# Kernel optimization log

Measured on AMD Instinct MI355X. Metric: run time of the kernel, lower is better.

The kernel has to match this reference:

```python
import jax, jax.numpy as jnp
import numpy as np

INPUT_SIZE = 2
HIDDEN = 64
NUM_CLASSES = 64
B = 4096
T = 512


def setup_inputs() -> dict:
    key = jax.random.key(0)
    ks = jax.random.split(key, 12)
    s_in = 1.0 / np.sqrt(HIDDEN)
    inp = {
        "x": jax.random.normal(ks[0], (B, INPUT_SIZE, T, 1), dtype=jnp.float32),
        # LSTMCell params (torch layout: [4H, in], gate order i,f,g,o)
        "W_ih": jax.random.uniform(ks[1], (4 * HIDDEN, INPUT_SIZE), minval=-s_in, maxval=s_in),
        "W_hh": jax.random.uniform(ks[2], (4 * HIDDEN, HIDDEN), minval=-s_in, maxval=s_in),
        "b_ih": jax.random.uniform(ks[3], (4 * HIDDEN,), minval=-s_in, maxval=s_in),
        "b_hh": jax.random.uniform(ks[4], (4 * HIDDEN,), minval=-s_in, maxval=s_in),
        # ODE cell f_node: Linear(H,H) -> Tanh -> Linear(H,H)
        "W1": jax.random.uniform(ks[5], (HIDDEN, HIDDEN), minval=-s_in, maxval=s_in),
        "b1": jax.random.uniform(ks[6], (HIDDEN,), minval=-s_in, maxval=s_in),
        "W2": jax.random.uniform(ks[7], (HIDDEN, HIDDEN), minval=-s_in, maxval=s_in),
        "b2": jax.random.uniform(ks[8], (HIDDEN,), minval=-s_in, maxval=s_in),
        # output projection fc
        "Wf": jax.random.uniform(ks[9], (NUM_CLASSES, HIDDEN), minval=-s_in, maxval=s_in),
        "bf": jax.random.uniform(ks[10], (NUM_CLASSES,), minval=-s_in, maxval=s_in),
    }
    return inp


def reference(x, W_ih, W_hh, b_ih, b_hh, W1, b1, W2, b2, Wf, bf):
    # x: [B, input_size, T, 1] -> [T, B, input_size] for scan over time
    xs = jnp.transpose(x[..., 0], (2, 0, 1))
    b = xs.shape[1]
    H = W_hh.shape[1]
    dt = jnp.float32(1.0 / 3.0)  # ts = ones(B), 3 fixed Euler steps of ts/3

    def f_node(h):
        return jnp.tanh(h @ W1.T + b1) @ W2.T + b2

    def step(carry, xt):
        h, c = carry
        gates = xt @ W_ih.T + h @ W_hh.T + (b_ih + b_hh)  # [B, 4H]
        i, f, g, o = jnp.split(gates, 4, axis=-1)
        c = jax.nn.sigmoid(f) * c + jax.nn.sigmoid(i) * jnp.tanh(g)
        h = jax.nn.sigmoid(o) * jnp.tanh(c)
        # fixed-Euler ODE solve: 3 steps
        for _ in range(3):
            h = h + dt * f_node(h)
        return (h, c), h @ Wf.T + bf

    h0 = jnp.zeros((b, H), dtype=x.dtype)
    c0 = jnp.zeros((b, H), dtype=x.dtype)
    _, outs = jax.lax.scan(step, (h0, c0), xs)  # outs: [T, B, num_classes]
    return jnp.transpose(outs, (1, 0, 2))  # [B, T, num_classes]
```

## Files before the change

### kernel.cpp

```cpp
#include <hip/hip_runtime.h>


#define TT 512
#define DT 0.33333334f

#define OFF_M  0
#define OFF_N  4096
#define OFF_P  20480
#define OFF_K1 24576
#define OFF_CG 24640
#define OFF_C2 24896

typedef _Float16 half8 __attribute__((ext_vector_type(8)));
typedef float f32x4 __attribute__((ext_vector_type(4)));

__device__ __forceinline__ float fsig(float x) {
  return __builtin_amdgcn_rcpf(1.0f + __expf(-x));
}
__device__ __forceinline__ float ftanh(float x) {
  return 2.0f * __builtin_amdgcn_rcpf(1.0f + __expf(-2.0f * x)) - 1.0f;
}

__global__ void prep(const float* __restrict__ Whh, const float* __restrict__ W1,
                     const float* __restrict__ W2, const float* __restrict__ b2,
                     const float* __restrict__ Wf, const float* __restrict__ bf,
                     float* __restrict__ ws) {
  int id = (int)blockIdx.x * 256 + (int)threadIdx.x;
  if (id < 4096) {
    int j = id >> 6, k = id & 63;
    float s = 0.f;
    for (int l = 0; l < 64; ++l) s += W1[j * 64 + l] * W2[l * 64 + k];
    ws[OFF_M + id] = DT * s;
  } else if (id < 20480) {
    int e = id - 4096; int gr = e >> 6, k = e & 63;
    float s = 0.f;
    for (int l = 0; l < 64; ++l) s += Whh[gr * 64 + l] * W2[l * 64 + k];
    ws[OFF_N + e] = DT * s;
  } else if (id < 24576) {
    int e = id - 20480; int j = e >> 6, k = e & 63;
    float s = 0.f;
    for (int l = 0; l < 64; ++l) s += Wf[j * 64 + l] * W2[l * 64 + k];
    ws[OFF_P + e] = DT * s;
  } else if (id < 24640) {
    int j = id - 24576;
    float s = 0.f;
    for (int l = 0; l < 64; ++l) s += W1[j * 64 + l] * b2[l];
    ws[OFF_K1 + j] = DT * s;
  } else if (id < 24896) {
    int gr = id - 24640;
    float s = 0.f;
    for (int l = 0; l < 64; ++l) s += Whh[gr * 64 + l] * b2[l];
    ws[OFF_CG + gr] = 3.0f * DT * s;
  } else if (id < 24960) {
    int j = id - 24896;
    float s = 0.f;
    for (int l = 0; l < 64; ++l) s += Wf[j * 64 + l] * b2[l];
    ws[OFF_C2 + j] = 3.0f * DT * s + bf[j];
  }
}

__device__ __forceinline__ half8 rdA(const _Float16* plane, int off) {
  return *(const half8*)(plane + off);
}

__global__ void __launch_bounds__(256, 1)
odelstm(const float* __restrict__ X, const float* __restrict__ Wih,
        const float* __restrict__ Whh, const float* __restrict__ bih,
        const float* __restrict__ bhh, const float* __restrict__ W1,
        const float* __restrict__ b1, const float* __restrict__ Wf,
        const float* __restrict__ ws, float* __restrict__ OUT)
{
  __shared__ __align__(16) _Float16 sh[5 * 1024];

  const int tid = (int)threadIdx.x;
  const int w = tid >> 6;
  const int l = tid & 63;
  const int q = l >> 4;
  const int p = l & 15;
  const int j = (w << 4) | p;
  const int row0 = (int)blockIdx.x << 4;

  half8 Bhh[4][2], Bw1[2], Bm[2], Bn[4][2], Bp[2], Bof[2];
  #pragma unroll
  for (int g = 0; g < 4; ++g) {
    #pragma unroll
    for (int kt = 0; kt < 2; ++kt) {
      const float* s  = Whh + ((g << 6) | j) * 64 + (kt << 5) + (q << 3);
      const float* sn = ws + OFF_N + (((g << 6) | j) << 6) + (kt << 5) + (q << 3);
      half8 v, vn;
      #pragma unroll
      for (int i = 0; i < 8; ++i) { v[i] = (_Float16)s[i]; vn[i] = (_Float16)sn[i]; }
      Bhh[g][kt] = v; Bn[g][kt] = vn;
    }
  }
  #pragma unroll
  for (int kt = 0; kt < 2; ++kt) {
    const float* s1 = W1 + j * 64 + (kt << 5) + (q << 3);
    const float* sm = ws + OFF_M + (j << 6) + (kt << 5) + (q << 3);
    const float* sp = ws + OFF_P + (j << 6) + (kt << 5) + (q << 3);
    const float* sf = Wf + j * 64 + (kt << 5) + (q << 3);
    half8 v1, vm, vp, vf;
    #pragma unroll
    for (int i = 0; i < 8; ++i) {
      v1[i] = (_Float16)s1[i]; vm[i] = (_Float16)sm[i];
      vp[i] = (_Float16)sp[i]; vf[i] = (_Float16)sf[i];
    }
    Bw1[kt] = v1; Bm[kt] = vm; Bp[kt] = vp; Bof[kt] = vf;
  }

  float bias0[4], biasL[4], wx0[4], wx1[4];
  #pragma unroll
  for (int g = 0; g < 4; ++g) {
    int gr = (g << 6) | j;
    bias0[g] = bih[gr] + bhh[gr];
    biasL[g] = bias0[g] + ws[OFF_CG + gr];
    wx0[g] = Wih[gr * 2];
    wx1[g] = Wih[gr * 2 + 1];
  }
  const float b1c = b1[j];
  const float k1c = ws[OFF_K1 + j];
  const float c2c = ws[OFF_C2 + j];

  int waddr[4];
  #pragma unroll
  for (int r = 0; r < 4; ++r) {
    int row = (q << 2) | r;
    waddr[r] = row * 64 + (((j >> 3) ^ (row & 7)) << 3) + (j & 7);
  }
  int roff0 = p * 64 + (((q) ^ (p & 7)) << 3);
  int roff1 = p * 64 + (((4 | q) ^ (p & 7)) << 3);

  const float* xp[4];
  float* outp[4];
  #pragma unroll
  for (int r = 0; r < 4; ++r) {
    int rb = row0 + ((q << 2) | r);
    xp[r]   = X + rb * 2 * TT;
    outp[r] = OUT + (rb * TT) * 64 + j;
  }

  float x0[4], x1[4];
  #pragma unroll
  for (int r = 0; r < 4; ++r) { x0[r] = xp[r][0]; x1[r] = xp[r][TT]; }

  f32x4 acc[4];
  #pragma unroll
  for (int g = 0; g < 4; ++g)
    #pragma unroll
    for (int r = 0; r < 4; ++r)
      acc[g][r] = bias0[g] + x0[r] * wx0[g] + x1[r] * wx1[g];

  float c[4] = {0.f, 0.f, 0.f, 0.f};

  for (int t = 0; t < TT; ++t) {
    _Float16* Hpl = sh + ((t & 1) << 10);
    _Float16* T0p = sh + 2048;
    _Float16* T1p = sh + 3072;
    _Float16* Spp = sh + 4096;

    float hd[4];
    #pragma unroll
    for (int r = 0; r < 4; ++r) {
      float ig = fsig(acc[0][r]);
      float fg = fsig(acc[1][r]);
      float gg = ftanh(acc[2][r]);
      float og = fsig(acc[3][r]);
      c[r]  = fg * c[r] + ig * gg;
      hd[r] = og * ftanh(c[r]);
      Hpl[waddr[r]] = (_Float16)hd[r];
    }
    __syncthreads();

    half8 hf0 = rdA(Hpl, roff0);
    half8 hf1 = rdA(Hpl, roff1);
    f32x4 aa = {b1c, b1c, b1c, b1c};
    aa = __builtin_amdgcn_mfma_f32_16x16x32_f16(hf0, Bw1[0], aa, 0, 0, 0);
    aa = __builtin_amdgcn_mfma_f32_16x16x32_f16(hf1, Bw1[1], aa, 0, 0, 0);

    int tn = (t + 1 < TT) ? t + 1 : t;
    float nx0[4], nx1[4];
    #pragma unroll
    for (int r = 0; r < 4; ++r) { nx0[r] = xp[r][tn]; nx1[r] = xp[r][TT + tn]; }

    float t0s[4];
    #pragma unroll
    for (int r = 0; r < 4; ++r) {
      t0s[r] = ftanh(aa[r]);
      T0p[waddr[r]] = (_Float16)t0s[r];
    }
    __syncthreads();
    half8 t0f0 = rdA(T0p, roff0);
    half8 t0f1 = rdA(T0p, roff1);
    f32x4 a1 = {aa[0] + k1c, aa[1] + k1c, aa[2] + k1c, aa[3] + k1c};
    a1 = __builtin_amdgcn_mfma_f32_16x16x32_f16(t0f0, Bm[0], a1, 0, 0, 0);
    a1 = __builtin_amdgcn_mfma_f32_16x16x32_f16(t0f1, Bm[1], a1, 0, 0, 0);

    float t1s[4];
    #pragma unroll
    for (int r = 0; r < 4; ++r) {
      t1s[r] = ftanh(a1[r]);
      T1p[waddr[r]] = (_Float16)t1s[r];
    }
    __syncthreads();
    half8 t1f0 = rdA(T1p, roff0);
    half8 t1f1 = rdA(T1p, roff1);
    f32x4 a2 = {a1[0] + k1c, a1[1] + k1c, a1[2] + k1c, a1[3] + k1c};
    a2 = __builtin_amdgcn_mfma_f32_16x16x32_f16(t1f0, Bm[0], a2, 0, 0, 0);
    a2 = __builtin_amdgcn_mfma_f32_16x16x32_f16(t1f1, Bm[1], a2, 0, 0, 0);

    #pragma unroll
    for (int r = 0; r < 4; ++r) {
      float Sv = t0s[r] + t1s[r] + ftanh(a2[r]);
      Spp[waddr[r]] = (_Float16)Sv;
    }
    __syncthreads();

    half8 sf0 = rdA(Spp, roff0);
    half8 sf1 = rdA(Spp, roff1);

    #pragma unroll
    for (int g = 0; g < 4; ++g) {
      #pragma unroll
      for (int r = 0; r < 4; ++r)
        acc[g][r] = biasL[g] + nx0[r] * wx0[g] + nx1[r] * wx1[g];
      acc[g] = __builtin_amdgcn_mfma_f32_16x16x32_f16(hf0, Bhh[g][0], acc[g], 0, 0, 0);
      acc[g] = __builtin_amdgcn_mfma_f32_16x16x32_f16(hf1, Bhh[g][1], acc[g], 0, 0, 0);
      acc[g] = __builtin_amdgcn_mfma_f32_16x16x32_f16(sf0, Bn[g][0],  acc[g], 0, 0, 0);
      acc[g] = __builtin_amdgcn_mfma_f32_16x16x32_f16(sf1, Bn[g][1],  acc[g], 0, 0, 0);
    }

    f32x4 oa = {c2c, c2c, c2c, c2c};
    oa = __builtin_amdgcn_mfma_f32_16x16x32_f16(hf0, Bof[0], oa, 0, 0, 0);
    oa = __builtin_amdgcn_mfma_f32_16x16x32_f16(hf1, Bof[1], oa, 0, 0, 0);
    oa = __builtin_amdgcn_mfma_f32_16x16x32_f16(sf0, Bp[0],  oa, 0, 0, 0);
    oa = __builtin_amdgcn_mfma_f32_16x16x32_f16(sf1, Bp[1],  oa, 0, 0, 0);

    #pragma unroll
    for (int r = 0; r < 4; ++r) {
      outp[r][0] = oa[r];
      outp[r] += 64;
    }

    #pragma unroll
    for (int r = 0; r < 4; ++r) { x0[r] = nx0[r]; x1[r] = nx1[r]; }
  }
}

extern "C" void kernel_launch(void* const* d_in, const int* in_sizes, int n_in,
                              void* d_out, int out_size, void* d_ws, size_t ws_size,
                              hipStream_t stream) {
  const float* X   = (const float*)d_in[0];
  const float* Wih = (const float*)d_in[1];
  const float* Whh = (const float*)d_in[2];
  const float* bih = (const float*)d_in[3];
  const float* bhh = (const float*)d_in[4];
  const float* W1  = (const float*)d_in[5];
  const float* b1  = (const float*)d_in[6];
  const float* W2  = (const float*)d_in[7];
  const float* b2  = (const float*)d_in[8];
  const float* Wf  = (const float*)d_in[9];
  const float* bf  = (const float*)d_in[10];
  float* OUT = (float*)d_out;
  float* ws  = (float*)d_ws;

  hipLaunchKernelGGL(prep, dim3(98), dim3(256), 0, stream,
                     Whh, W1, W2, b2, Wf, bf, ws);

  int B = in_sizes[0] / (2 * TT);
  dim3 grid(B / 16), block(256);
  hipLaunchKernelGGL(odelstm, grid, block, 0, stream,
                     X, Wih, Whh, bih, bhh, W1, b1, Wf, ws, OUT);
}
```

Before: 1.190 ms.

## Halve rows per block and run two blocks per CU to hide recurrence latency

Each block now handles 8 batch rows instead of 16, so twice as many blocks are launched, and launch bounds allow two blocks per CU. The 16-row MFMA tiles stay the same size: the unused rows come from zero-initialised shared memory and zeroed accumulator lanes. The aim is to interleave two independent serial recurrence chains on each CU, hiding MFMA, LDS and barrier latency. In exchange, half of each MFMA's work is padding and weight registers are loaded per block twice as often.

```diff
diff --git a/kernel.cpp b/kernel.cpp
--- a/kernel.cpp
+++ b/kernel.cpp
@@ -63,7 +63,7 @@
   return *(const half8*)(plane + off);
 }
 
-__global__ void __launch_bounds__(256, 1)
+__global__ void __launch_bounds__(256, 2)
 odelstm(const float* __restrict__ X, const float* __restrict__ Wih,
         const float* __restrict__ Whh, const float* __restrict__ bih,
         const float* __restrict__ bhh, const float* __restrict__ W1,
@@ -78,7 +78,7 @@
   const int q = l >> 4;
   const int p = l & 15;
   const int j = (w << 4) | p;
-  const int row0 = (int)blockIdx.x << 4;
+  const int row0 = (int)blockIdx.x << 3;
 
   half8 Bhh[4][2], Bw1[2], Bm[2], Bn[4][2], Bp[2], Bof[2];
   #pragma unroll
@@ -121,36 +121,41 @@
   const float k1c = ws[OFF_K1 + j];
   const float c2c = ws[OFF_C2 + j];
 
-  int waddr[4];
-  #pragma unroll
-  for (int r = 0; r < 4; ++r) {
+  int waddr[2];
+  #pragma unroll
+  for (int r = 0; r < 2; ++r) {
     int row = (q << 2) | r;
     waddr[r] = row * 64 + (((j >> 3) ^ (row & 7)) << 3) + (j & 7);
   }
   int roff0 = p * 64 + (((q) ^ (p & 7)) << 3);
   int roff1 = p * 64 + (((4 | q) ^ (p & 7)) << 3);
 
-  const float* xp[4];
-  float* outp[4];
-  #pragma unroll
-  for (int r = 0; r < 4; ++r) {
-    int rb = row0 + ((q << 2) | r);
+  const float* xp[2];
+  float* outp[2];
+  #pragma unroll
+  for (int r = 0; r < 2; ++r) {
+    int rb = row0 + ((q << 1) | r);
     xp[r]   = X + rb * 2 * TT;
     outp[r] = OUT + (rb * TT) * 64 + j;
   }
 
-  float x0[4], x1[4];
-  #pragma unroll
-  for (int r = 0; r < 4; ++r) { x0[r] = xp[r][0]; x1[r] = xp[r][TT]; }
+  for (int i = tid; i < 5 * 1024; i += 256) sh[i] = (_Float16)0.f;
+
+  float x0[2], x1[2];
+  #pragma unroll
+  for (int r = 0; r < 2; ++r) { x0[r] = xp[r][0]; x1[r] = xp[r][TT]; }
 
   f32x4 acc[4];
   #pragma unroll
-  for (int g = 0; g < 4; ++g)
-    #pragma unroll
-    for (int r = 0; r < 4; ++r)
-      acc[g][r] = bias0[g] + x0[r] * wx0[g] + x1[r] * wx1[g];
-
-  float c[4] = {0.f, 0.f, 0.f, 0.f};
+  for (int g = 0; g < 4; ++g) {
+    acc[g][0] = bias0[g] + x0[0] * wx0[g] + x1[0] * wx1[g];
+    acc[g][1] = bias0[g] + x0[1] * wx0[g] + x1[1] * wx1[g];
+    acc[g][2] = 0.f; acc[g][3] = 0.f;
+  }
+
+  float c[2] = {0.f, 0.f};
+
+  __syncthreads();
 
   for (int t = 0; t < TT; ++t) {
     _Float16* Hpl = sh + ((t & 1) << 10);
@@ -158,16 +163,15 @@
     _Float16* T1p = sh + 3072;
     _Float16* Spp = sh + 4096;
 
-    float hd[4];
-    #pragma unroll
-    for (int r = 0; r < 4; ++r) {
+    #pragma unroll
+    for (int r = 0; r < 2; ++r) {
       float ig = fsig(acc[0][r]);
       float fg = fsig(acc[1][r]);
       float gg = ftanh(acc[2][r]);
       float og = fsig(acc[3][r]);
-      c[r]  = fg * c[r] + ig * gg;
-      hd[r] = og * ftanh(c[r]);
-      Hpl[waddr[r]] = (_Float16)hd[r];
+      c[r] = fg * c[r] + ig * gg;
+      float hv = og * ftanh(c[r]);
+      Hpl[waddr[r]] = (_Float16)hv;
     }
     __syncthreads();
 
@@ -178,38 +182,38 @@
     aa = __builtin_amdgcn_mfma_f32_16x16x32_f16(hf1, Bw1[1], aa, 0, 0, 0);
 
     int tn = (t + 1 < TT) ? t + 1 : t;
-    float nx0[4], nx1[4];
-    #pragma unroll
-    for (int r = 0; r < 4; ++r) { nx0[r] = xp[r][tn]; nx1[r] = xp[r][TT + tn]; }
-
-    float t0s[4];
-    #pragma unroll
-    for (int r = 0; r < 4; ++r) {
+    float nx0[2], nx1[2];
+    #pragma unroll
+    for (int r = 0; r < 2; ++r) { nx0[r] = xp[r][tn]; nx1[r] = xp[r][TT + tn]; }
+
+    float t0s[2];
+    #pragma unroll
+    for (int r = 0; r < 2; ++r) {
       t0s[r] = ftanh(aa[r]);
       T0p[waddr[r]] = (_Float16)t0s[r];
     }
     __syncthreads();
     half8 t0f0 = rdA(T0p, roff0);
     half8 t0f1 = rdA(T0p, roff1);
-    f32x4 a1 = {aa[0] + k1c, aa[1] + k1c, aa[2] + k1c, aa[3] + k1c};
+    f32x4 a1 = {aa[0] + k1c, aa[1] + k1c, 0.f, 0.f};
     a1 = __builtin_amdgcn_mfma_f32_16x16x32_f16(t0f0, Bm[0], a1, 0, 0, 0);
     a1 = __builtin_amdgcn_mfma_f32_16x16x32_f16(t0f1, Bm[1], a1, 0, 0, 0);
 
-    float t1s[4];
-    #pragma unroll
-    for (int r = 0; r < 4; ++r) {
+    float t1s[2];
+    #pragma unroll
+    for (int r = 0; r < 2; ++r) {
       t1s[r] = ftanh(a1[r]);
       T1p[waddr[r]] = (_Float16)t1s[r];
     }
     __syncthreads();
     half8 t1f0 = rdA(T1p, roff0);
     half8 t1f1 = rdA(T1p, roff1);
-    f32x4 a2 = {a1[0] + k1c, a1[1] + k1c, a1[2] + k1c, a1[3] + k1c};
+    f32x4 a2 = {a1[0] + k1c, a1[1] + k1c, 0.f, 0.f};
     a2 = __builtin_amdgcn_mfma_f32_16x16x32_f16(t1f0, Bm[0], a2, 0, 0, 0);
     a2 = __builtin_amdgcn_mfma_f32_16x16x32_f16(t1f1, Bm[1], a2, 0, 0, 0);
 
     #pragma unroll
-    for (int r = 0; r < 4; ++r) {
+    for (int r = 0; r < 2; ++r) {
       float Sv = t0s[r] + t1s[r] + ftanh(a2[r]);
       Spp[waddr[r]] = (_Float16)Sv;
     }
@@ -220,29 +224,29 @@
 
     #pragma unroll
     for (int g = 0; g < 4; ++g) {
-      #pragma unroll
-      for (int r = 0; r < 4; ++r)
-        acc[g][r] = biasL[g] + nx0[r] * wx0[g] + nx1[r] * wx1[g];
+      acc[g][0] = biasL[g] + nx0[0] * wx0[g] + nx1[0] * wx1[g];
+      acc[g][1] = biasL[g] + nx0[1] * wx0[g] + nx1[1] * wx1[g];
+      acc[g][2] = 0.f; acc[g][3] = 0.f;
       acc[g] = __builtin_amdgcn_mfma_f32_16x16x32_f16(hf0, Bhh[g][0], acc[g], 0, 0, 0);
       acc[g] = __builtin_amdgcn_mfma_f32_16x16x32_f16(hf1, Bhh[g][1], acc[g], 0, 0, 0);
       acc[g] = __builtin_amdgcn_mfma_f32_16x16x32_f16(sf0, Bn[g][0],  acc[g], 0, 0, 0);
       acc[g] = __builtin_amdgcn_mfma_f32_16x16x32_f16(sf1, Bn[g][1],  acc[g], 0, 0, 0);
     }
 
-    f32x4 oa = {c2c, c2c, c2c, c2c};
+    f32x4 oa = {c2c, c2c, 0.f, 0.f};
     oa = __builtin_amdgcn_mfma_f32_16x16x32_f16(hf0, Bof[0], oa, 0, 0, 0);
     oa = __builtin_amdgcn_mfma_f32_16x16x32_f16(hf1, Bof[1], oa, 0, 0, 0);
     oa = __builtin_amdgcn_mfma_f32_16x16x32_f16(sf0, Bp[0],  oa, 0, 0, 0);
     oa = __builtin_amdgcn_mfma_f32_16x16x32_f16(sf1, Bp[1],  oa, 0, 0, 0);
 
     #pragma unroll
-    for (int r = 0; r < 4; ++r) {
+    for (int r = 0; r < 2; ++r) {
       outp[r][0] = oa[r];
       outp[r] += 64;
     }
 
     #pragma unroll
-    for (int r = 0; r < 4; ++r) { x0[r] = nx0[r]; x1[r] = nx1[r]; }
+    for (int r = 0; r < 2; ++r) { x0[r] = nx0[r]; x1[r] = nx1[r]; }
   }
 }
 
@@ -267,7 +271,7 @@
                      Whh, W1, W2, b2, Wf, bf, ws);
 
   int B = in_sizes[0] / (2 * TT);
-  dim3 grid(B / 16), block(256);
+  dim3 grid(B / 8), block(256);
   hipLaunchKernelGGL(odelstm, grid, block, 0, stream,
                      X, Wih, Whh, bih, bhh, W1, b1, Wf, ws, OUT);
 }
```

After: 1.076 ms. -9.6%, faster.
